# Optimization experiments

Hardware: AMD Instinct MI355X
Metric: run time of the kernel (lower is better)

## Reference

```python
import jax, jax.numpy as jnp
import numpy as np

D_MODEL = 2816
N_HEADS = 16
DH = 512
N_KV = 2
MAX_CTX = 8192
POS = 4095  # current decode position (0-indexed)
EPS = 1e-6
Q_DIM = N_HEADS * DH
KV_DIM = N_KV * DH
NEG_INF = -1e9


def setup_inputs() -> dict:
    key = jax.random.key(0)
    ks = jax.random.split(key, 8)
    x = jax.random.normal(ks[0], (1, 1, D_MODEL), jnp.float32)
    # Realistic RoPE angles at position POS (full head_dim rotation, half/half layout)
    inv_freq = 1.0 / (10000.0 ** (np.arange(0, DH, 2, dtype=np.float32) / DH))  # (DH/2,)
    ang = POS * inv_freq
    cos = jnp.asarray(np.concatenate([np.cos(ang), np.cos(ang)])[None, None, :], jnp.float32)  # (1,1,DH)
    sin = jnp.asarray(np.concatenate([np.sin(ang), np.sin(ang)])[None, None, :], jnp.float32)
    k_cache = jax.random.normal(ks[1], (1, N_KV, MAX_CTX, DH), jnp.float32) * 0.02
    v_cache = jax.random.normal(ks[2], (1, N_KV, MAX_CTX, DH), jnp.float32) * 0.02
    # causal decode mask: attend to [0, POS], -inf beyond
    pos_ids = jnp.arange(MAX_CTX)
    attn_mask = jnp.where(pos_ids <= POS, 0.0, NEG_INF).astype(jnp.float32).reshape(1, 1, 1, MAX_CTX)
    # one-hot write mask at current position
    kv_write_mask = jnp.zeros((1, 1, MAX_CTX, 1), jnp.float32).at[0, 0, POS, 0].set(1.0)
    Wq = jax.random.normal(ks[3], (Q_DIM, D_MODEL), jnp.float32) * 0.02
    Wk = jax.random.normal(ks[4], (KV_DIM, D_MODEL), jnp.float32) * 0.02
    Wo = jax.random.normal(ks[5], (D_MODEL, Q_DIM), jnp.float32) * 0.02
    q_gamma = jax.random.normal(ks[6], (DH,), jnp.float32) * 0.02  # stored as (gamma-1)
    k_gamma = jax.random.normal(ks[7], (DH,), jnp.float32) * 0.02
    return {"x": x, "cos": cos, "sin": sin, "k_cache": k_cache, "v_cache": v_cache,
            "attn_mask": attn_mask, "kv_write_mask": kv_write_mask,
            "Wq": Wq, "Wk": Wk, "Wo": Wo, "q_gamma": q_gamma, "k_gamma": k_gamma}


def _rmsnorm(x, w=None):
    v = jnp.mean(x * x, axis=-1, keepdims=True)
    x = x * jax.lax.rsqrt(v + EPS)
    return x if w is None else x * (1.0 + w)


def _rope(x, cos, sin):
    # x: (1,T,H,D); cos/sin: (1,T,D)
    c = cos[:, :, None, :]
    s = sin[:, :, None, :]
    d = x.shape[-1]
    x1, x2 = x[..., : d // 2], x[..., d // 2 :]
    rot = jnp.concatenate([-x2, x1], axis=-1)
    return x * c + rot * s


def reference(x, cos, sin, k_cache, v_cache, attn_mask, kv_write_mask, Wq, Wk, Wo, q_gamma, k_gamma):
    q_raw = (x @ Wq.T).reshape(1, 1, N_HEADS, DH)
    k_raw = (x @ Wk.T).reshape(1, 1, N_KV, DH)
    q = _rope(_rmsnorm(q_raw, q_gamma), cos, sin)
    k = _rope(_rmsnorm(k_raw, k_gamma), cos, sin)
    v = _rmsnorm(k_raw)  # unscaled norm, not rotated
    q = jnp.swapaxes(q, 1, 2)  # (1,H,1,D)
    k = jnp.swapaxes(k, 1, 2)  # (1,n_kv,1,D)
    v = jnp.swapaxes(v, 1, 2)
    k_new = k_cache + k * kv_write_mask  # broadcast write at current slot
    v_new = v_cache + v * kv_write_mask
    rep = N_HEADS // N_KV
    K = jnp.repeat(k_new, rep, axis=1)  # (1,H,S,D)
    V = jnp.repeat(v_new, rep, axis=1)
    scores = jnp.einsum("bhtd,bhsd->bhts", q, K) + attn_mask  # no 1/sqrt(d) scale, as in source
    w = jax.nn.softmax(scores.astype(jnp.float32), axis=-1).astype(q.dtype)
    ctx = jnp.einsum("bhts,bhsd->bhtd", w, V)  # (1,H,1,D)
    ctx = jnp.swapaxes(ctx, 1, 2).reshape(1, 1, Q_DIM)
    out = ctx @ Wo.T
    return (out, k_new, v_new)
```

## Files before the change

kernel.cpp:

```cpp
#include <hip/hip_runtime.h>
#include <math.h>

#define D_MODEL 2816
#define N_HEADS 16
#define DH      512
#define N_KV    2
#define MAX_CTX 8192
#define POS     4095
#define EPS     1e-6f
#define Q_DIM   8192
#define KV_DIM  1024
#define GROUP   8
#define NPOS    4096
#define AB      128


__device__ __forceinline__ float4 f4_mul(float4 a, float s) {
  return make_float4(a.x*s, a.y*s, a.z*s, a.w*s);
}
__device__ __forceinline__ float4 f4_mul4(float4 a, float4 b) {
  return make_float4(a.x*b.x, a.y*b.y, a.z*b.z, a.w*b.w);
}
__device__ __forceinline__ float4 f4_fma(float4 a, float4 b, float4 c) {
  return make_float4(fmaf(a.x,b.x,c.x), fmaf(a.y,b.y,c.y), fmaf(a.z,b.z,c.z), fmaf(a.w,b.w,c.w));
}
__device__ __forceinline__ float4 f4_fmas(float s, float4 b, float4 c) {
  return make_float4(fmaf(s,b.x,c.x), fmaf(s,b.y,c.y), fmaf(s,b.z,c.z), fmaf(s,b.w,c.w));
}
__device__ __forceinline__ float4 f4_fnma(float4 a, float4 b, float4 c) {
  return make_float4(fmaf(-a.x,b.x,c.x), fmaf(-a.y,b.y,c.y), fmaf(-a.z,b.z,c.z), fmaf(-a.w,b.w,c.w));
}
__device__ __forceinline__ float4 f4_add(float4 a, float4 b) {
  return make_float4(a.x+b.x, a.y+b.y, a.z+b.z, a.w+b.w);
}
__device__ __forceinline__ float f4_dot(float4 a, float4 b) {
  return a.x*b.x + a.y*b.y + a.z*b.z + a.w*b.w;
}
__device__ __forceinline__ float f4_ssq(float4 a) {
  return a.x*a.x + a.y*a.y + a.z*a.z + a.w*a.w;
}

__global__ __launch_bounds__(256) void k_qkv(const float* __restrict__ x,
    const float* __restrict__ Wq, const float* __restrict__ Wk,
    float* __restrict__ qraw, float* __restrict__ kraw) {
  int wid  = (blockIdx.x * blockDim.x + threadIdx.x) >> 6;
  int lane = threadIdx.x & 63;
  const float4* x4 = (const float4*)x;
  int row = wid;
  const float4* W4 = (row < Q_DIM)
      ? (const float4*)(Wq + (size_t)row * D_MODEL)
      : (const float4*)(Wk + (size_t)(row - Q_DIM) * D_MODEL);
  float acc0 = 0.f, acc1 = 0.f;
#pragma unroll
  for (int it = 0; it < D_MODEL / 256; ++it) {
    float4 w  = W4[it * 64 + lane];
    float4 xv = x4[it * 64 + lane];
    float d = f4_dot(w, xv);
    if (it & 1) acc1 += d; else acc0 += d;
  }
  float acc = acc0 + acc1;
#pragma unroll
  for (int m = 32; m; m >>= 1) acc += __shfl_xor(acc, m, 64);
  if (lane == 0) {
    if (row < Q_DIM) qraw[row] = acc;
    else             kraw[row - Q_DIM] = acc;
  }
}

__global__ __launch_bounds__(512) void k_fused(
    const float* __restrict__ kc, const float* __restrict__ vc,
    const float* __restrict__ qraw, const float* __restrict__ kraw,
    const float* __restrict__ cosv, const float* __restrict__ sinv,
    const float* __restrict__ qg,   const float* __restrict__ kg,
    float* __restrict__ knew, float* __restrict__ vnew,
    float* __restrict__ part, float* __restrict__ lpart) {
  __shared__ float4 lq[GROUP * 128];
  __shared__ float  pvbuf[8 * 512];
  __shared__ float  lbuf[64];
  __shared__ float4 kfin[128];
  __shared__ float4 vfin[128];
  int b = blockIdx.x;
  int g = b >> 8;
  int rb = b & 255;
  int t = threadIdx.x;
  int w = t >> 6, lane = t & 63;
  bool att = (rb < AB);

  if (att) {
    const float4* c4 = (const float4*)cosv;
    const float4* s4 = (const float4*)sinv;
    float4 c1 = c4[lane],      s1 = s4[lane];
    float4 c2 = c4[64 + lane], s2 = s4[64 + lane];
    const float4* qr4 = (const float4*)(qraw + (size_t)(g * GROUP + w) * DH);
    float4 a  = qr4[lane];
    float4 b2 = qr4[64 + lane];
    float ss = f4_ssq(a) + f4_ssq(b2);
#pragma unroll
    for (int m = 32; m; m >>= 1) ss += __shfl_xor(ss, m, 64);
    float scale = rsqrtf(ss * (1.f / (float)DH) + EPS);
    const float4* qg4 = (const float4*)qg;
    float4 ga = qg4[lane], gb = qg4[64 + lane];
    float4 na = f4_mul4(f4_mul(a,  scale), make_float4(1.f+ga.x,1.f+ga.y,1.f+ga.z,1.f+ga.w));
    float4 nb = f4_mul4(f4_mul(b2, scale), make_float4(1.f+gb.x,1.f+gb.y,1.f+gb.z,1.f+gb.w));
    lq[w * 128 + lane]      = f4_fnma(nb, s1, f4_mul4(na, c1));
    lq[w * 128 + 64 + lane] = f4_fma (na, s2, f4_mul4(nb, c2));
    if (rb == (POS >> 5) && w == 0) {
      const float4* kr4 = (const float4*)(kraw + (size_t)g * DH);
      float4 ka_ = kr4[lane];
      float4 kb_ = kr4[64 + lane];
      float ss2 = f4_ssq(ka_) + f4_ssq(kb_);
#pragma unroll
      for (int m = 32; m; m >>= 1) ss2 += __shfl_xor(ss2, m, 64);
      float sc2 = rsqrtf(ss2 * (1.f / (float)DH) + EPS);
      float4 va_ = f4_mul(ka_, sc2);
      float4 vb_ = f4_mul(kb_, sc2);
      const float4* kg4 = (const float4*)kg;
      float4 ga2 = kg4[lane], gb2 = kg4[64 + lane];
      float4 na2 = f4_mul4(va_, make_float4(1.f+ga2.x,1.f+ga2.y,1.f+ga2.z,1.f+ga2.w));
      float4 nb2 = f4_mul4(vb_, make_float4(1.f+gb2.x,1.f+gb2.y,1.f+gb2.z,1.f+gb2.w));
      kfin[lane]      = f4_fnma(nb2, s1, f4_mul4(na2, c1));
      kfin[64 + lane] = f4_fma (na2, s2, f4_mul4(nb2, c2));
      vfin[lane]      = va_;
      vfin[64 + lane] = vb_;
    }
  }
  __syncthreads();

  float4 acc[GROUP][2];
#pragma unroll
  for (int h = 0; h < GROUP; ++h) { acc[h][0] = make_float4(0,0,0,0); acc[h][1] = make_float4(0,0,0,0); }
  float lacc[GROUP] = {0.f,0.f,0.f,0.f,0.f,0.f,0.f,0.f};

  for (int r = 0; r < 4; ++r) {
    int s = (rb << 5) + (w << 2) + r;
    size_t row = ((size_t)g * MAX_CTX + s) * DH;
    const float4* kc4 = (const float4*)(kc + row);
    const float4* vc4 = (const float4*)(vc + row);
    float4 ka = kc4[lane], kb = kc4[64 + lane];
    float4 va = vc4[lane], vb = vc4[64 + lane];
    if (s == POS) {
      ka = f4_add(ka, kfin[lane]); kb = f4_add(kb, kfin[64 + lane]);
      va = f4_add(va, vfin[lane]); vb = f4_add(vb, vfin[64 + lane]);
    }
    float4* ko4 = (float4*)(knew + row);
    float4* vo4 = (float4*)(vnew + row);
    ko4[lane] = ka; ko4[64 + lane] = kb;
    vo4[lane] = va; vo4[64 + lane] = vb;
    if (att) {
      float sc[GROUP];
#pragma unroll
      for (int h = 0; h < GROUP; ++h)
        sc[h] = f4_dot(lq[h * 128 + lane], ka) + f4_dot(lq[h * 128 + 64 + lane], kb);
#pragma unroll
      for (int h = 0; h < GROUP; ++h) {
#pragma unroll
        for (int m = 32; m; m >>= 1) sc[h] += __shfl_xor(sc[h], m, 64);
      }
#pragma unroll
      for (int h = 0; h < GROUP; ++h) {
        float e = __expf(fminf(sc[h], 80.f));
        lacc[h] += e;
        acc[h][0] = f4_fmas(e, va, acc[h][0]);
        acc[h][1] = f4_fmas(e, vb, acc[h][1]);
      }
    }
  }

  if (att) {
    float4* pv4 = (float4*)pvbuf;
#pragma unroll
    for (int h = 0; h < GROUP; ++h) {
      __syncthreads();
      pv4[w * 128 + lane]      = acc[h][0];
      pv4[w * 128 + 64 + lane] = acc[h][1];
      __syncthreads();
      float sum = 0.f;
#pragma unroll
      for (int w2 = 0; w2 < 8; ++w2) sum += pvbuf[w2 * 512 + t];
      part[((size_t)(g * AB + rb)) * (GROUP * DH) + h * 512 + t] = sum;
    }
    float myl = 0.f;
#pragma unroll
    for (int h = 0; h < GROUP; ++h) myl = (lane == h) ? lacc[h] : myl;
    if (lane < 8) lbuf[w * 8 + lane] = myl;
    __syncthreads();
    if (t < 8) {
      float sl = 0.f;
#pragma unroll
      for (int w2 = 0; w2 < 8; ++w2) sl += lbuf[w2 * 8 + t];
      lpart[(g * AB + rb) * 8 + t] = sl;
    }
  }
}

__global__ __launch_bounds__(256) void k_reduce_ctx(
    const float* __restrict__ part, const float* __restrict__ lpart,
    float* __restrict__ ctx) {
  int hd = blockIdx.x * 256 + threadIdx.x;
  int h = hd >> 9;
  int g = h >> 3, hh = h & 7;
  const float* p  = part  + (size_t)g * AB * (GROUP * DH) + hh * 512 + (hd & 511);
  const float* lp = lpart + g * AB * 8 + hh;
  float acc = 0.f, l = 0.f;
  for (int c = 0; c < AB; ++c) {
    acc += p[(size_t)c * (GROUP * DH)];
    l   += lp[c * 8];
  }
  ctx[hd] = acc / l;
}

__global__ __launch_bounds__(256) void k_oproj(const float* __restrict__ ctx,
    const float* __restrict__ Wo, float* __restrict__ out) {
  int wid  = (blockIdx.x * blockDim.x + threadIdx.x) >> 6;
  int lane = threadIdx.x & 63;
  const float4* c4 = (const float4*)ctx;
  int row = wid;
  const float4* W4 = (const float4*)(Wo + (size_t)row * Q_DIM);
  float acc0 = 0.f, acc1 = 0.f;
#pragma unroll
  for (int it = 0; it < Q_DIM / 256; ++it) {
    float4 w  = W4[it * 64 + lane];
    float4 cv = c4[it * 64 + lane];
    float d = f4_dot(w, cv);
    if (it & 1) acc1 += d; else acc0 += d;
  }
  float acc = acc0 + acc1;
#pragma unroll
  for (int m = 32; m; m >>= 1) acc += __shfl_xor(acc, m, 64);
  if (lane == 0) out[row] = acc;
}

extern "C" void kernel_launch(void* const* d_in, const int* in_sizes, int n_in,
                              void* d_out, int out_size, void* d_ws, size_t ws_size,
                              hipStream_t stream) {
  (void)in_sizes; (void)n_in; (void)out_size; (void)ws_size;
  const float* x    = (const float*)d_in[0];
  const float* cosv = (const float*)d_in[1];
  const float* sinv = (const float*)d_in[2];
  const float* kc   = (const float*)d_in[3];
  const float* vc   = (const float*)d_in[4];
  const float* Wq   = (const float*)d_in[7];
  const float* Wk   = (const float*)d_in[8];
  const float* Wo   = (const float*)d_in[9];
  const float* qg   = (const float*)d_in[10];
  const float* kg   = (const float*)d_in[11];

  float* out  = (float*)d_out;
  float* knew = out + D_MODEL;
  float* vnew = knew + (size_t)N_KV * MAX_CTX * DH;

  float* w      = (float*)d_ws;
  float* qraw   = w;
  float* kraw   = w + 8192;
  float* part   = w + 9216;
  float* lpart  = w + 1057792;
  float* ctx    = w + 1059840;

  k_qkv       <<<2304, 256, 0, stream>>>(x, Wq, Wk, qraw, kraw);
  k_fused     <<<512, 512, 0, stream>>>(kc, vc, qraw, kraw, cosv, sinv, qg, kg,
                                        knew, vnew, part, lpart);
  k_reduce_ctx<<<32, 256, 0, stream>>>(part, lpart, ctx);
  k_oproj     <<<704, 256, 0, stream>>>(ctx, Wo, out);
}
```

Before: 79.18 us.

## Merge four kernels into one persistent megakernel with grid barriers

Replaces the four launches (QKV projection, fused attention and cache copy, context reduce, output projection) with one persistent kernel of 256 blocks separated by atomic grid-wide barriers. Each block handles two attention/copy work units, and the output projection splits each row across two waves. The aim is to remove inter-kernel launch gaps and tail bubbles. In exchange it adds a memset, spin-wait barriers, lower parallelism in the projection phases, and a hang risk if not all 256 blocks are co-resident.

```diff
diff --git a/kernel.cpp b/kernel.cpp
--- a/kernel.cpp
+++ b/kernel.cpp
@@ -13,6 +13,8 @@
 #define GROUP   8
 #define NPOS    4096
 #define AB      128
+#define NBLK    256
+#define NWAVE   2048
 
 
 __device__ __forceinline__ float4 f4_mul(float4 a, float s) {
@@ -40,194 +42,217 @@
   return a.x*a.x + a.y*a.y + a.z*a.z + a.w*a.w;
 }
 
-__global__ __launch_bounds__(256) void k_qkv(const float* __restrict__ x,
-    const float* __restrict__ Wq, const float* __restrict__ Wk,
-    float* __restrict__ qraw, float* __restrict__ kraw) {
-  int wid  = (blockIdx.x * blockDim.x + threadIdx.x) >> 6;
-  int lane = threadIdx.x & 63;
-  const float4* x4 = (const float4*)x;
-  int row = wid;
-  const float4* W4 = (row < Q_DIM)
-      ? (const float4*)(Wq + (size_t)row * D_MODEL)
-      : (const float4*)(Wk + (size_t)(row - Q_DIM) * D_MODEL);
-  float acc0 = 0.f, acc1 = 0.f;
-#pragma unroll
-  for (int it = 0; it < D_MODEL / 256; ++it) {
-    float4 w  = W4[it * 64 + lane];
-    float4 xv = x4[it * 64 + lane];
-    float d = f4_dot(w, xv);
-    if (it & 1) acc1 += d; else acc0 += d;
-  }
-  float acc = acc0 + acc1;
-#pragma unroll
-  for (int m = 32; m; m >>= 1) acc += __shfl_xor(acc, m, 64);
-  if (lane == 0) {
-    if (row < Q_DIM) qraw[row] = acc;
-    else             kraw[row - Q_DIM] = acc;
-  }
-}
-
-__global__ __launch_bounds__(512) void k_fused(
-    const float* __restrict__ kc, const float* __restrict__ vc,
-    const float* __restrict__ qraw, const float* __restrict__ kraw,
+__device__ __forceinline__ void gridbar(int* cnt, int id) {
+  __syncthreads();
+  if (threadIdx.x == 0) {
+    __hip_atomic_fetch_add(&cnt[id], 1, __ATOMIC_ACQ_REL, __HIP_MEMORY_SCOPE_AGENT);
+    while (__hip_atomic_load(&cnt[id], __ATOMIC_ACQUIRE, __HIP_MEMORY_SCOPE_AGENT) < NBLK)
+      __builtin_amdgcn_s_sleep(1);
+  }
+  __syncthreads();
+}
+
+__global__ __launch_bounds__(512) void k_mega(
+    const float* __restrict__ x,
     const float* __restrict__ cosv, const float* __restrict__ sinv,
+    const float* __restrict__ kc,   const float* __restrict__ vc,
+    const float* __restrict__ Wq,   const float* __restrict__ Wk,
+    const float* __restrict__ Wo,
     const float* __restrict__ qg,   const float* __restrict__ kg,
-    float* __restrict__ knew, float* __restrict__ vnew,
-    float* __restrict__ part, float* __restrict__ lpart) {
+    float* __restrict__ out, float* __restrict__ knew, float* __restrict__ vnew,
+    float* __restrict__ qraw_ctx, float* __restrict__ kraw,
+    float* __restrict__ part, float* __restrict__ lpart, int* __restrict__ cnt) {
   __shared__ float4 lq[GROUP * 128];
   __shared__ float  pvbuf[8 * 512];
   __shared__ float  lbuf[64];
   __shared__ float4 kfin[128];
   __shared__ float4 vfin[128];
-  int b = blockIdx.x;
-  int g = b >> 8;
-  int rb = b & 255;
+  __shared__ float  rsum[8];
+
   int t = threadIdx.x;
   int w = t >> 6, lane = t & 63;
-  bool att = (rb < AB);
-
-  if (att) {
-    const float4* c4 = (const float4*)cosv;
-    const float4* s4 = (const float4*)sinv;
-    float4 c1 = c4[lane],      s1 = s4[lane];
-    float4 c2 = c4[64 + lane], s2 = s4[64 + lane];
-    const float4* qr4 = (const float4*)(qraw + (size_t)(g * GROUP + w) * DH);
-    float4 a  = qr4[lane];
-    float4 b2 = qr4[64 + lane];
-    float ss = f4_ssq(a) + f4_ssq(b2);
-#pragma unroll
-    for (int m = 32; m; m >>= 1) ss += __shfl_xor(ss, m, 64);
-    float scale = rsqrtf(ss * (1.f / (float)DH) + EPS);
-    const float4* qg4 = (const float4*)qg;
-    float4 ga = qg4[lane], gb = qg4[64 + lane];
-    float4 na = f4_mul4(f4_mul(a,  scale), make_float4(1.f+ga.x,1.f+ga.y,1.f+ga.z,1.f+ga.w));
-    float4 nb = f4_mul4(f4_mul(b2, scale), make_float4(1.f+gb.x,1.f+gb.y,1.f+gb.z,1.f+gb.w));
-    lq[w * 128 + lane]      = f4_fnma(nb, s1, f4_mul4(na, c1));
-    lq[w * 128 + 64 + lane] = f4_fma (na, s2, f4_mul4(nb, c2));
-    if (rb == (POS >> 5) && w == 0) {
-      const float4* kr4 = (const float4*)(kraw + (size_t)g * DH);
-      float4 ka_ = kr4[lane];
-      float4 kb_ = kr4[64 + lane];
-      float ss2 = f4_ssq(ka_) + f4_ssq(kb_);
-#pragma unroll
-      for (int m = 32; m; m >>= 1) ss2 += __shfl_xor(ss2, m, 64);
-      float sc2 = rsqrtf(ss2 * (1.f / (float)DH) + EPS);
-      float4 va_ = f4_mul(ka_, sc2);
-      float4 vb_ = f4_mul(kb_, sc2);
-      const float4* kg4 = (const float4*)kg;
-      float4 ga2 = kg4[lane], gb2 = kg4[64 + lane];
-      float4 na2 = f4_mul4(va_, make_float4(1.f+ga2.x,1.f+ga2.y,1.f+ga2.z,1.f+ga2.w));
-      float4 nb2 = f4_mul4(vb_, make_float4(1.f+gb2.x,1.f+gb2.y,1.f+gb2.z,1.f+gb2.w));
-      kfin[lane]      = f4_fnma(nb2, s1, f4_mul4(na2, c1));
-      kfin[64 + lane] = f4_fma (na2, s2, f4_mul4(nb2, c2));
-      vfin[lane]      = va_;
-      vfin[64 + lane] = vb_;
-    }
-  }
-  __syncthreads();
-
-  float4 acc[GROUP][2];
-#pragma unroll
-  for (int h = 0; h < GROUP; ++h) { acc[h][0] = make_float4(0,0,0,0); acc[h][1] = make_float4(0,0,0,0); }
-  float lacc[GROUP] = {0.f,0.f,0.f,0.f,0.f,0.f,0.f,0.f};
-
-  for (int r = 0; r < 4; ++r) {
-    int s = (rb << 5) + (w << 2) + r;
-    size_t row = ((size_t)g * MAX_CTX + s) * DH;
-    const float4* kc4 = (const float4*)(kc + row);
-    const float4* vc4 = (const float4*)(vc + row);
-    float4 ka = kc4[lane], kb = kc4[64 + lane];
-    float4 va = vc4[lane], vb = vc4[64 + lane];
-    if (s == POS) {
-      ka = f4_add(ka, kfin[lane]); kb = f4_add(kb, kfin[64 + lane]);
-      va = f4_add(va, vfin[lane]); vb = f4_add(vb, vfin[64 + lane]);
-    }
-    float4* ko4 = (float4*)(knew + row);
-    float4* vo4 = (float4*)(vnew + row);
-    ko4[lane] = ka; ko4[64 + lane] = kb;
-    vo4[lane] = va; vo4[64 + lane] = vb;
+  int blk = blockIdx.x;
+  int W = blk * 8 + w;
+
+  {
+    const float4* x4 = (const float4*)x;
+    for (int row = W; row < Q_DIM + KV_DIM; row += NWAVE) {
+      const float4* W4 = (row < Q_DIM)
+          ? (const float4*)(Wq + (size_t)row * D_MODEL)
+          : (const float4*)(Wk + (size_t)(row - Q_DIM) * D_MODEL);
+      float a0 = 0.f, a1 = 0.f;
+#pragma unroll
+      for (int it = 0; it < D_MODEL / 256; ++it) {
+        float d = f4_dot(W4[it * 64 + lane], x4[it * 64 + lane]);
+        if (it & 1) a1 += d; else a0 += d;
+      }
+      float acc = a0 + a1;
+#pragma unroll
+      for (int m = 32; m; m >>= 1) acc += __shfl_xor(acc, m, 64);
+      if (lane == 0) {
+        if (row < Q_DIM) qraw_ctx[row] = acc;
+        else             kraw[row - Q_DIM] = acc;
+      }
+    }
+  }
+  gridbar(cnt, 0);
+
+  for (int ui = 0; ui < 2; ++ui) {
+    int u = ui ? (511 - blk) : blk;
+    int g = u >> 8;
+    int rb = u & 255;
+    bool att = (rb < AB);
+
     if (att) {
-      float sc[GROUP];
-#pragma unroll
-      for (int h = 0; h < GROUP; ++h)
-        sc[h] = f4_dot(lq[h * 128 + lane], ka) + f4_dot(lq[h * 128 + 64 + lane], kb);
+      const float4* c4 = (const float4*)cosv;
+      const float4* s4 = (const float4*)sinv;
+      float4 c1 = c4[lane],      s1 = s4[lane];
+      float4 c2 = c4[64 + lane], s2 = s4[64 + lane];
+      const float4* qr4 = (const float4*)(qraw_ctx + (size_t)(g * GROUP + w) * DH);
+      float4 a  = qr4[lane];
+      float4 b2 = qr4[64 + lane];
+      float ss = f4_ssq(a) + f4_ssq(b2);
+#pragma unroll
+      for (int m = 32; m; m >>= 1) ss += __shfl_xor(ss, m, 64);
+      float scale = rsqrtf(ss * (1.f / (float)DH) + EPS);
+      const float4* qg4 = (const float4*)qg;
+      float4 ga = qg4[lane], gb = qg4[64 + lane];
+      float4 na = f4_mul4(f4_mul(a,  scale), make_float4(1.f+ga.x,1.f+ga.y,1.f+ga.z,1.f+ga.w));
+      float4 nb = f4_mul4(f4_mul(b2, scale), make_float4(1.f+gb.x,1.f+gb.y,1.f+gb.z,1.f+gb.w));
+      lq[w * 128 + lane]      = f4_fnma(nb, s1, f4_mul4(na, c1));
+      lq[w * 128 + 64 + lane] = f4_fma (na, s2, f4_mul4(nb, c2));
+      if (rb == (POS >> 5) && w == 0) {
+        const float4* kr4 = (const float4*)(kraw + (size_t)g * DH);
+        float4 ka_ = kr4[lane];
+        float4 kb_ = kr4[64 + lane];
+        float ss2 = f4_ssq(ka_) + f4_ssq(kb_);
+#pragma unroll
+        for (int m = 32; m; m >>= 1) ss2 += __shfl_xor(ss2, m, 64);
+        float sc2 = rsqrtf(ss2 * (1.f / (float)DH) + EPS);
+        float4 va_ = f4_mul(ka_, sc2);
+        float4 vb_ = f4_mul(kb_, sc2);
+        const float4* kg4 = (const float4*)kg;
+        float4 ga2 = kg4[lane], gb2 = kg4[64 + lane];
+        float4 na2 = f4_mul4(va_, make_float4(1.f+ga2.x,1.f+ga2.y,1.f+ga2.z,1.f+ga2.w));
+        float4 nb2 = f4_mul4(vb_, make_float4(1.f+gb2.x,1.f+gb2.y,1.f+gb2.z,1.f+gb2.w));
+        kfin[lane]      = f4_fnma(nb2, s1, f4_mul4(na2, c1));
+        kfin[64 + lane] = f4_fma (na2, s2, f4_mul4(nb2, c2));
+        vfin[lane]      = va_;
+        vfin[64 + lane] = vb_;
+      }
+      __syncthreads();
+    }
+
+    float4 acc[GROUP][2];
+#pragma unroll
+    for (int h = 0; h < GROUP; ++h) { acc[h][0] = make_float4(0,0,0,0); acc[h][1] = make_float4(0,0,0,0); }
+    float lacc[GROUP] = {0.f,0.f,0.f,0.f,0.f,0.f,0.f,0.f};
+
+    for (int r = 0; r < 4; ++r) {
+      int s = (rb << 5) + (w << 2) + r;
+      size_t row = ((size_t)g * MAX_CTX + s) * DH;
+      const float4* kc4 = (const float4*)(kc + row);
+      const float4* vc4 = (const float4*)(vc + row);
+      float4 ka = kc4[lane], kb = kc4[64 + lane];
+      float4 va = vc4[lane], vb = vc4[64 + lane];
+      if (s == POS) {
+        ka = f4_add(ka, kfin[lane]); kb = f4_add(kb, kfin[64 + lane]);
+        va = f4_add(va, vfin[lane]); vb = f4_add(vb, vfin[64 + lane]);
+      }
+      float4* ko4 = (float4*)(knew + row);
+      float4* vo4 = (float4*)(vnew + row);
+      ko4[lane] = ka; ko4[64 + lane] = kb;
+      vo4[lane] = va; vo4[64 + lane] = vb;
+      if (att) {
+        float sc[GROUP];
+#pragma unroll
+        for (int h = 0; h < GROUP; ++h)
+          sc[h] = f4_dot(lq[h * 128 + lane], ka) + f4_dot(lq[h * 128 + 64 + lane], kb);
+#pragma unroll
+        for (int h = 0; h < GROUP; ++h) {
+#pragma unroll
+          for (int m = 32; m; m >>= 1) sc[h] += __shfl_xor(sc[h], m, 64);
+        }
+#pragma unroll
+        for (int h = 0; h < GROUP; ++h) {
+          float e = __expf(fminf(sc[h], 80.f));
+          lacc[h] += e;
+          acc[h][0] = f4_fmas(e, va, acc[h][0]);
+          acc[h][1] = f4_fmas(e, vb, acc[h][1]);
+        }
+      }
+    }
+
+    if (att) {
+      float4* pv4 = (float4*)pvbuf;
 #pragma unroll
       for (int h = 0; h < GROUP; ++h) {
-#pragma unroll
-        for (int m = 32; m; m >>= 1) sc[h] += __shfl_xor(sc[h], m, 64);
-      }
-#pragma unroll
-      for (int h = 0; h < GROUP; ++h) {
-        float e = __expf(fminf(sc[h], 80.f));
-        lacc[h] += e;
-        acc[h][0] = f4_fmas(e, va, acc[h][0]);
-        acc[h][1] = f4_fmas(e, vb, acc[h][1]);
-      }
-    }
-  }
-
-  if (att) {
-    float4* pv4 = (float4*)pvbuf;
-#pragma unroll
-    for (int h = 0; h < GROUP; ++h) {
-      __syncthreads();
-      pv4[w * 128 + lane]      = acc[h][0];
-      pv4[w * 128 + 64 + lane] = acc[h][1];
-      __syncthreads();
-      float sum = 0.f;
-#pragma unroll
-      for (int w2 = 0; w2 < 8; ++w2) sum += pvbuf[w2 * 512 + t];
-      part[((size_t)(g * AB + rb)) * (GROUP * DH) + h * 512 + t] = sum;
-    }
-    float myl = 0.f;
-#pragma unroll
-    for (int h = 0; h < GROUP; ++h) myl = (lane == h) ? lacc[h] : myl;
-    if (lane < 8) lbuf[w * 8 + lane] = myl;
-    __syncthreads();
-    if (t < 8) {
-      float sl = 0.f;
-#pragma unroll
-      for (int w2 = 0; w2 < 8; ++w2) sl += lbuf[w2 * 8 + t];
-      lpart[(g * AB + rb) * 8 + t] = sl;
-    }
-  }
-}
-
-__global__ __launch_bounds__(256) void k_reduce_ctx(
-    const float* __restrict__ part, const float* __restrict__ lpart,
-    float* __restrict__ ctx) {
-  int hd = blockIdx.x * 256 + threadIdx.x;
-  int h = hd >> 9;
-  int g = h >> 3, hh = h & 7;
-  const float* p  = part  + (size_t)g * AB * (GROUP * DH) + hh * 512 + (hd & 511);
-  const float* lp = lpart + g * AB * 8 + hh;
-  float acc = 0.f, l = 0.f;
-  for (int c = 0; c < AB; ++c) {
-    acc += p[(size_t)c * (GROUP * DH)];
-    l   += lp[c * 8];
-  }
-  ctx[hd] = acc / l;
-}
-
-__global__ __launch_bounds__(256) void k_oproj(const float* __restrict__ ctx,
-    const float* __restrict__ Wo, float* __restrict__ out) {
-  int wid  = (blockIdx.x * blockDim.x + threadIdx.x) >> 6;
-  int lane = threadIdx.x & 63;
-  const float4* c4 = (const float4*)ctx;
-  int row = wid;
-  const float4* W4 = (const float4*)(Wo + (size_t)row * Q_DIM);
-  float acc0 = 0.f, acc1 = 0.f;
-#pragma unroll
-  for (int it = 0; it < Q_DIM / 256; ++it) {
-    float4 w  = W4[it * 64 + lane];
-    float4 cv = c4[it * 64 + lane];
-    float d = f4_dot(w, cv);
-    if (it & 1) acc1 += d; else acc0 += d;
-  }
-  float acc = acc0 + acc1;
-#pragma unroll
-  for (int m = 32; m; m >>= 1) acc += __shfl_xor(acc, m, 64);
-  if (lane == 0) out[row] = acc;
+        __syncthreads();
+        pv4[w * 128 + lane]      = acc[h][0];
+        pv4[w * 128 + 64 + lane] = acc[h][1];
+        __syncthreads();
+        float sum = 0.f;
+#pragma unroll
+        for (int w2 = 0; w2 < 8; ++w2) sum += pvbuf[w2 * 512 + t];
+        part[((size_t)(g * AB + rb)) * (GROUP * DH) + h * 512 + t] = sum;
+      }
+      float myl = 0.f;
+#pragma unroll
+      for (int h = 0; h < GROUP; ++h) myl = (lane == h) ? lacc[h] : myl;
+      if (lane < 8) lbuf[w * 8 + lane] = myl;
+      __syncthreads();
+      if (t < 8) {
+        float sl = 0.f;
+#pragma unroll
+        for (int w2 = 0; w2 < 8; ++w2) sl += lbuf[w2 * 8 + t];
+        lpart[(g * AB + rb) * 8 + t] = sl;
+      }
+    }
+  }
+  gridbar(cnt, 1);
+
+  if (blk < 64 && t < 128) {
+    int hd = blk * 128 + t;
+    int g  = hd >> 12;
+    int hh = (hd >> 9) & 7;
+    int d  = hd & 511;
+    const float* p  = part  + (size_t)(g * AB) * (GROUP * DH) + hh * 512 + d;
+    const float* lp = lpart + g * AB * 8 + hh;
+    float acc = 0.f, l = 0.f;
+    for (int c = 0; c < AB; ++c) {
+      acc += p[(size_t)c * (GROUP * DH)];
+      l   += lp[c * 8];
+    }
+    qraw_ctx[hd] = acc / l;
+  }
+  gridbar(cnt, 2);
+
+  {
+    const float4* c4 = (const float4*)qraw_ctx;
+    for (int p = 0; p < 3; ++p) {
+      int row = p * 1024 + blk * 4 + (w >> 1);
+      bool valid = (row < D_MODEL);
+      float acc = 0.f;
+      if (valid) {
+        const float4* W4 = (const float4*)(Wo + (size_t)row * Q_DIM);
+        int it0 = (w & 1) * 16;
+        float a0 = 0.f, a1 = 0.f;
+#pragma unroll
+        for (int i = 0; i < 16; ++i) {
+          int it = it0 + i;
+          float d = f4_dot(W4[it * 64 + lane], c4[it * 64 + lane]);
+          if (i & 1) a1 += d; else a0 += d;
+        }
+        acc = a0 + a1;
+#pragma unroll
+        for (int m = 32; m; m >>= 1) acc += __shfl_xor(acc, m, 64);
+        if (lane == 0) rsum[w] = acc;
+      }
+      __syncthreads();
+      if (valid && (w & 1) == 0 && lane == 0) out[row] = rsum[w] + rsum[w + 1];
+      __syncthreads();
+    }
+  }
 }
 
 extern "C" void kernel_launch(void* const* d_in, const int* in_sizes, int n_in,
@@ -249,16 +274,14 @@
   float* knew = out + D_MODEL;
   float* vnew = knew + (size_t)N_KV * MAX_CTX * DH;
 
-  float* w      = (float*)d_ws;
-  float* qraw   = w;
-  float* kraw   = w + 8192;
-  float* part   = w + 9216;
-  float* lpart  = w + 1057792;
-  float* ctx    = w + 1059840;
-
-  k_qkv       <<<2304, 256, 0, stream>>>(x, Wq, Wk, qraw, kraw);
-  k_fused     <<<512, 512, 0, stream>>>(kc, vc, qraw, kraw, cosv, sinv, qg, kg,
-                                        knew, vnew, part, lpart);
-  k_reduce_ctx<<<32, 256, 0, stream>>>(part, lpart, ctx);
-  k_oproj     <<<704, 256, 0, stream>>>(ctx, Wo, out);
-}
+  float* w        = (float*)d_ws;
+  float* qraw_ctx = w;
+  float* kraw     = w + 8192;
+  float* part     = w + 9216;
+  float* lpart    = w + 1057792;
+  int*   cnt      = (int*)(w + 1059840);
+
+  hipMemsetAsync(cnt, 0, 3 * sizeof(int), stream);
+  k_mega<<<NBLK, 512, 0, stream>>>(x, cosv, sinv, kc, vc, Wq, Wk, Wo, qg, kg,
+                                   out, knew, vnew, qraw_ctx, kraw, part, lpart, cnt);
+}
```

New measurement: 159.2 us. 2.01x slower.

## Replace split-K partial buffers and reduce kernel with atomic accumulation

Applied to the files above, without the earlier changes.

The attention kernel now atomically adds each block's per-head context partials and softmax denominators straight into a small ctx/lvec buffer, which is zeroed in the first block of the QKV kernel. The separate reduction kernel and its large partial-buffer round trip go away. The division by the denominator moves into the output projection through a per-head reciprocal held in shared memory. The cost is float atomic contention (128 blocks per address) and a non-deterministic summation order. The __syncthreads is also moved inside the att branch, which is safe only because the branch condition is uniform across the block.

```diff
diff --git a/kernel.cpp b/kernel.cpp
--- a/kernel.cpp
+++ b/kernel.cpp
@@ -42,23 +42,29 @@
 
 __global__ __launch_bounds__(256) void k_qkv(const float* __restrict__ x,
     const float* __restrict__ Wq, const float* __restrict__ Wk,
-    float* __restrict__ qraw, float* __restrict__ kraw) {
-  int wid  = (blockIdx.x * blockDim.x + threadIdx.x) >> 6;
-  int lane = threadIdx.x & 63;
+    float* __restrict__ qraw, float* __restrict__ kraw,
+    float* __restrict__ ctx, float* __restrict__ lvec) {
+  int t = threadIdx.x;
+  if (blockIdx.x == 0) {
+    float4* c4 = (float4*)ctx;
+#pragma unroll
+    for (int j = 0; j < 8; ++j) c4[j * 256 + t] = make_float4(0.f, 0.f, 0.f, 0.f);
+    if (t < 16) lvec[t] = 0.f;
+  }
+  int wid  = (blockIdx.x * blockDim.x + t) >> 6;
+  int lane = t & 63;
   const float4* x4 = (const float4*)x;
   int row = wid;
   const float4* W4 = (row < Q_DIM)
       ? (const float4*)(Wq + (size_t)row * D_MODEL)
       : (const float4*)(Wk + (size_t)(row - Q_DIM) * D_MODEL);
-  float acc0 = 0.f, acc1 = 0.f;
+  float a0 = 0.f, a1 = 0.f;
 #pragma unroll
   for (int it = 0; it < D_MODEL / 256; ++it) {
-    float4 w  = W4[it * 64 + lane];
-    float4 xv = x4[it * 64 + lane];
-    float d = f4_dot(w, xv);
-    if (it & 1) acc1 += d; else acc0 += d;
-  }
-  float acc = acc0 + acc1;
+    float d = f4_dot(W4[it * 64 + lane], x4[it * 64 + lane]);
+    if (it & 1) a1 += d; else a0 += d;
+  }
+  float acc = a0 + a1;
 #pragma unroll
   for (int m = 32; m; m >>= 1) acc += __shfl_xor(acc, m, 64);
   if (lane == 0) {
@@ -73,7 +79,7 @@
     const float* __restrict__ cosv, const float* __restrict__ sinv,
     const float* __restrict__ qg,   const float* __restrict__ kg,
     float* __restrict__ knew, float* __restrict__ vnew,
-    float* __restrict__ part, float* __restrict__ lpart) {
+    float* __restrict__ ctx, float* __restrict__ lvec) {
   __shared__ float4 lq[GROUP * 128];
   __shared__ float  pvbuf[8 * 512];
   __shared__ float  lbuf[64];
@@ -123,8 +129,8 @@
       vfin[lane]      = va_;
       vfin[64 + lane] = vb_;
     }
-  }
-  __syncthreads();
+    __syncthreads();
+  }
 
   float4 acc[GROUP][2];
 #pragma unroll
@@ -177,7 +183,7 @@
       float sum = 0.f;
 #pragma unroll
       for (int w2 = 0; w2 < 8; ++w2) sum += pvbuf[w2 * 512 + t];
-      part[((size_t)(g * AB + rb)) * (GROUP * DH) + h * 512 + t] = sum;
+      atomicAdd(&ctx[(size_t)(g * GROUP + h) * DH + t], sum);
     }
     float myl = 0.f;
 #pragma unroll
@@ -188,43 +194,30 @@
       float sl = 0.f;
 #pragma unroll
       for (int w2 = 0; w2 < 8; ++w2) sl += lbuf[w2 * 8 + t];
-      lpart[(g * AB + rb) * 8 + t] = sl;
-    }
-  }
-}
-
-__global__ __launch_bounds__(256) void k_reduce_ctx(
-    const float* __restrict__ part, const float* __restrict__ lpart,
-    float* __restrict__ ctx) {
-  int hd = blockIdx.x * 256 + threadIdx.x;
-  int h = hd >> 9;
-  int g = h >> 3, hh = h & 7;
-  const float* p  = part  + (size_t)g * AB * (GROUP * DH) + hh * 512 + (hd & 511);
-  const float* lp = lpart + g * AB * 8 + hh;
-  float acc = 0.f, l = 0.f;
-  for (int c = 0; c < AB; ++c) {
-    acc += p[(size_t)c * (GROUP * DH)];
-    l   += lp[c * 8];
-  }
-  ctx[hd] = acc / l;
+      atomicAdd(&lvec[g * GROUP + t], sl);
+    }
+  }
 }
 
 __global__ __launch_bounds__(256) void k_oproj(const float* __restrict__ ctx,
-    const float* __restrict__ Wo, float* __restrict__ out) {
-  int wid  = (blockIdx.x * blockDim.x + threadIdx.x) >> 6;
-  int lane = threadIdx.x & 63;
+    const float* __restrict__ lvec, const float* __restrict__ Wo,
+    float* __restrict__ out) {
+  __shared__ float linv[16];
+  int t = threadIdx.x;
+  if (t < 16) linv[t] = 1.f / lvec[t];
+  __syncthreads();
+  int wid  = (blockIdx.x * blockDim.x + t) >> 6;
+  int lane = t & 63;
   const float4* c4 = (const float4*)ctx;
   int row = wid;
   const float4* W4 = (const float4*)(Wo + (size_t)row * Q_DIM);
-  float acc0 = 0.f, acc1 = 0.f;
+  float a0 = 0.f, a1 = 0.f;
 #pragma unroll
   for (int it = 0; it < Q_DIM / 256; ++it) {
-    float4 w  = W4[it * 64 + lane];
-    float4 cv = c4[it * 64 + lane];
-    float d = f4_dot(w, cv);
-    if (it & 1) acc1 += d; else acc0 += d;
-  }
-  float acc = acc0 + acc1;
+    float d = f4_dot(W4[it * 64 + lane], c4[it * 64 + lane]) * linv[it >> 1];
+    if (it & 1) a1 += d; else a0 += d;
+  }
+  float acc = a0 + a1;
 #pragma unroll
   for (int m = 32; m; m >>= 1) acc += __shfl_xor(acc, m, 64);
   if (lane == 0) out[row] = acc;
@@ -252,13 +245,11 @@
   float* w      = (float*)d_ws;
   float* qraw   = w;
   float* kraw   = w + 8192;
-  float* part   = w + 9216;
-  float* lpart  = w + 1057792;
-  float* ctx    = w + 1059840;
-
-  k_qkv       <<<2304, 256, 0, stream>>>(x, Wq, Wk, qraw, kraw);
-  k_fused     <<<512, 512, 0, stream>>>(kc, vc, qraw, kraw, cosv, sinv, qg, kg,
-                                        knew, vnew, part, lpart);
-  k_reduce_ctx<<<32, 256, 0, stream>>>(part, lpart, ctx);
-  k_oproj     <<<704, 256, 0, stream>>>(ctx, Wo, out);
-}
+  float* ctx    = w + 9216;
+  float* lvec   = w + 17408;
+
+  k_qkv  <<<2304, 256, 0, stream>>>(x, Wq, Wk, qraw, kraw, ctx, lvec);
+  k_fused<<<512, 512, 0, stream>>>(kc, vc, qraw, kraw, cosv, sinv, qg, kg,
+                                   knew, vnew, ctx, lvec);
+  k_oproj<<<704, 256, 0, stream>>>(ctx, lvec, Wo, out);
+}
```

Measured after the change: 72.24 us. 8.8% less time.
